# Optimization experiments

Hardware: AMD Instinct MI355X
Metric: run time of the kernel (lower is better)

## Reference

```python
import jax, jax.numpy as jnp
import numpy as np

N_INT = 16384
N_BND = 4096
DIM_X = 3
NUM_RES = 8
NUM_FC = 3
D = 128


def _dim_net(x, wf, bf, Wres, bres, Wl, bl, lo, hi):
    # x: scalar coordinate for one input dimension; returns scalar u-component
    h = (2.0 * (x - lo) / (hi - lo) - 1.0) * wf + bf  # fc_first: Linear(1,D) -> [D]

    def block(h, p):
        W, b = p  # W: [NUM_FC, D, D], b: [NUM_FC, D]
        g = h
        for l in range(NUM_FC):
            g = g @ W[l] + b[l]
            if l != NUM_FC - 1:
                g = jnp.sin(g)
        return jnp.sin(g + h), None

    h, _ = jax.lax.scan(block, h, (Wres, bres))
    return (h @ Wl + bl)[0]  # fc_last: Linear(D,1) -> scalar


_d2_net = jax.grad(jax.grad(_dim_net, argnums=0), argnums=0)

# vmap over points (axis 0 of x) then over dims (axis 1 of X / axis 0 of params)
_vals = jax.vmap(jax.vmap(_dim_net, in_axes=(0,) + (None,) * 8),
                 in_axes=(1,) + (0,) * 8)
_d2s = jax.vmap(jax.vmap(_d2_net, in_axes=(0,) + (None,) * 8),
                in_axes=(1,) + (0,) * 8)


def setup_inputs() -> dict:
    key = jax.random.key(0)
    ks = jax.random.split(key, 5)
    X = jax.random.uniform(ks[0], (N_INT + N_BND, DIM_X), dtype=jnp.float32)
    rhs = jax.random.normal(ks[1], (N_INT + N_BND, 1), dtype=jnp.float32)
    w_first = 0.2 * jax.random.normal(ks[2], (DIM_X, D), dtype=jnp.float32)
    b_first = jnp.zeros((DIM_X, D), jnp.float32)
    W_res = jax.random.normal(ks[3], (DIM_X, NUM_RES, NUM_FC, D, D),
                              dtype=jnp.float32) / jnp.sqrt(jnp.float32(D))
    b_res = jnp.zeros((DIM_X, NUM_RES, NUM_FC, D), jnp.float32)
    W_last = jax.random.normal(ks[4], (DIM_X, D, 1),
                               dtype=jnp.float32) / jnp.sqrt(jnp.float32(D))
    b_last = jnp.zeros((DIM_X, 1), jnp.float32)
    lb = jnp.zeros((DIM_X,), jnp.float32)
    ub = jnp.ones((DIM_X,), jnp.float32)
    return {"X": X, "rhs": rhs, "w_first": w_first, "b_first": b_first,
            "W_res": W_res, "b_res": b_res, "W_last": W_last, "b_last": b_last,
            "lb": lb, "ub": ub}


def reference(X, rhs, w_first, b_first, W_res, b_res, W_last, b_last, lb, ub):
    Xi = X[:N_INT]          # interior points
    Xb = X[N_INT:]          # boundary points

    # Separable network: u(x) = prod_i f_i(x_i), so
    # Laplace u = sum_i f_i''(x_i) * prod_{j!=i} f_j(x_j)  (same math as double autograd)
    F = _vals(Xi, w_first, b_first, W_res, b_res, W_last, b_last, lb, ub)   # [DIM_X, N_INT]
    F2 = _d2s(Xi, w_first, b_first, W_res, b_res, W_last, b_last, lb, ub)   # [DIM_X, N_INT]

    lap = jnp.zeros_like(F[0])
    for i in range(DIM_X):
        p = F2[i]
        for j in range(DIM_X):
            if j != i:
                p = p * F[j]
        lap = lap + p

    equation = -lap[:, None] - rhs[:N_INT]

    Fb = _vals(Xb, w_first, b_first, W_res, b_res, W_last, b_last, lb, ub)  # [DIM_X, N_BND]
    u_b = jnp.prod(Fb, axis=0)[:, None]
    boundary = u_b - rhs[N_INT:]
    return equation, boundary
```

## Files before the change

### kernel.cpp

```cpp
#include <hip/hip_runtime.h>

#define N_INT 16384
#define NPTS  20480
#define DIMX  3
#define NRES  8
#define NFC   3
#define DD    128
#define Q     8
#define WPW   4
#define TPB   (WPW*64)
#define TILES_PER_DIM (NPTS/Q)
#define INT_TILES     (N_INT/Q)
#define NLAYER (DIMX*NRES*NFC)
#define MT 2
#define NT 8
#define KS 4

typedef unsigned int   u32;
typedef unsigned short u16;
typedef _Float16 f16;
typedef f16   f16x8 __attribute__((ext_vector_type(8)));
typedef float f32x4 __attribute__((ext_vector_type(4)));
typedef float v2f   __attribute__((ext_vector_type(2)));
typedef float v4f   __attribute__((ext_vector_type(4)));

__device__ __forceinline__ u32 pack_split(float x) {
    f16 h = (f16)x;
    f16 l = (f16)(x - (float)h);
    union { f16 f; u16 u; } a, b;
    a.f = h; b.f = l;
    return (u32)a.u | ((u32)b.u << 16);
}

__device__ __forceinline__ int aidx(int row, int feat) {
    return row*DD + (feat ^ (((row >> 1) & 7) << 3));
}

#define PKFMA_LO(ACC, W2, X2) \
  asm("v_pk_fma_f32 %0, %1, %2, %0 op_sel:[0,0,0] op_sel_hi:[1,0,1]" \
      : "+v"(ACC) : "v"(W2), "v"(X2))
#define PKFMA_HI(ACC, W2, X2) \
  asm("v_pk_fma_f32 %0, %1, %2, %0 op_sel:[0,1,0] op_sel_hi:[1,1,1]" \
      : "+v"(ACC) : "v"(W2), "v"(X2))

__global__ void pack_w(const float* __restrict__ W_res,
                       f16* __restrict__ Whi, f16* __restrict__ Wlo)
{
    int t = blockIdx.x*256 + threadIdx.x;
    if (t >= NLAYER*KS*NT*64) return;
    int lane = t & 63;
    int nt   = (t >> 6) & 7;
    int ks   = (t >> 9) & 3;
    int L    = t >> 11;
    int n = nt*16 + (lane & 15);
    size_t src = (size_t)L*DD*DD + (size_t)(ks*32 + (lane >> 4)*8)*DD + n;
    f16x8 vh, vl;
#pragma unroll
    for (int i = 0; i < 8; ++i) {
        float w = W_res[src + (size_t)i*DD];
        f16 hh = (f16)w;
        vh[i] = hh;
        vl[i] = (f16)(w - (float)hh);
    }
    ((f16x8*)Whi)[t] = vh;
    ((f16x8*)Wlo)[t] = vl;
}

__global__ __launch_bounds__(TPB, 2) void pinn_main(
    const float* __restrict__ X,
    const float* __restrict__ w_first,
    const float* __restrict__ b_first,
    const float* __restrict__ W_res,
    const float* __restrict__ b_res,
    const float* __restrict__ W_last,
    const float* __restrict__ b_last,
    const float* __restrict__ lb,
    const float* __restrict__ ub,
    const f16* __restrict__ Whi,
    const f16* __restrict__ Wlo,
    float* __restrict__ Fout,
    float* __restrict__ F2out)
{
    __shared__ u32 ldsA[WPW][32*DD];
    const int wave = threadIdx.x >> 6;
    const int lane = threadIdx.x & 63;
    const int gw   = blockIdx.x * WPW + wave;
    const int dim  = gw / TILES_PER_DIM;
    const int tile = gw % TILES_PER_DIM;
    const int p0   = tile * Q;

    const float lo = lb[dim], hi = ub[dim];
    const float sc = 2.0f / (hi - lo);
    const float blv = b_last[dim];
    const float* bp0 = b_res + (size_t)dim*(NRES*NFC*DD);

    if (tile < INT_TILES) {
        u32* A = ldsA[wave];
        const int g = lane >> 4;
        const int c = lane & 15;
        const f16x8* WHp = (const f16x8*)Whi;
        const f16x8* WLp = (const f16x8*)Wlo;

        float hv_[MT][NT], hd_[MT][NT], hdd_[MT][NT];
        float wfv[NT], bfv[NT], blw[NT];
        float tq[MT];
#pragma unroll
        for (int mt = 0; mt < MT; ++mt) {
            int q = 4*mt + g;
            float x = X[(p0 + q)*DIMX + dim];
            tq[mt] = fmaf(x - lo, sc, -1.0f);
        }
#pragma unroll
        for (int nt = 0; nt < NT; ++nt) {
            int f = nt*16 + c;
            wfv[nt] = w_first[dim*DD + f];
            bfv[nt] = b_first[dim*DD + f];
            blw[nt] = W_last[dim*DD + f];
        }
#pragma unroll
        for (int mt = 0; mt < MT; ++mt)
#pragma unroll
            for (int nt = 0; nt < NT; ++nt) {
                hv_[mt][nt]  = fmaf(tq[mt], wfv[nt], bfv[nt]);
                hd_[mt][nt]  = sc * wfv[nt];
                hdd_[mt][nt] = 0.f;
            }

        const int Lbase = dim * NRES * NFC;
        const float* bp = bp0;

#pragma unroll 1
        for (int r = 0; r < NRES; ++r) {
#pragma unroll
            for (int mt = 0; mt < MT; ++mt)
#pragma unroll
                for (int nt = 0; nt < NT; ++nt) {
                    int row = mt*16 + 4*g;
                    int f   = nt*16 + c;
                    A[aidx(row+0, f)] = pack_split(hv_[mt][nt]);
                    A[aidx(row+1, f)] = pack_split(hd_[mt][nt]);
                    A[aidx(row+2, f)] = pack_split(hdd_[mt][nt]);
                }

#pragma unroll 1
            for (int l = 0; l < NFC; ++l) {
                const int L = Lbase + r*NFC + l;
                f32x4 acc[MT][NT];
#pragma unroll
                for (int mt = 0; mt < MT; ++mt)
#pragma unroll
                    for (int nt = 0; nt < NT; ++nt)
                        acc[mt][nt] = (f32x4){0.f, 0.f, 0.f, 0.f};

#pragma unroll 1
                for (int ks = 0; ks < KS; ++ks) {
                    f16x8 ah[MT], al[MT];
#pragma unroll
                    for (int mt = 0; mt < MT; ++mt) {
                        int idx = aidx(mt*16 + c, ks*32 + g*8);
                        const uint4 A0 = *(const uint4*)&A[idx];
                        const uint4 A1 = *(const uint4*)&A[idx + 4];
                        union { u32 u[4]; f16x8 v; } ch, cl;
                        ch.u[0] = (A0.x & 0xFFFFu) | (A0.y << 16);
                        ch.u[1] = (A0.z & 0xFFFFu) | (A0.w << 16);
                        ch.u[2] = (A1.x & 0xFFFFu) | (A1.y << 16);
                        ch.u[3] = (A1.z & 0xFFFFu) | (A1.w << 16);
                        cl.u[0] = (A0.x >> 16) | (A0.y & 0xFFFF0000u);
                        cl.u[1] = (A0.z >> 16) | (A0.w & 0xFFFF0000u);
                        cl.u[2] = (A1.x >> 16) | (A1.y & 0xFFFF0000u);
                        cl.u[3] = (A1.z >> 16) | (A1.w & 0xFFFF0000u);
                        ah[mt] = ch.v;  al[mt] = cl.v;
                    }
                    const f16x8* whb = WHp + (size_t)((L*KS + ks)*NT)*64;
                    const f16x8* wlb = WLp + (size_t)((L*KS + ks)*NT)*64;
#pragma unroll
                    for (int nt = 0; nt < NT; ++nt) {
                        f16x8 bh = whb[nt*64 + lane];
                        f16x8 bl = wlb[nt*64 + lane];
#pragma unroll
                        for (int mt = 0; mt < MT; ++mt) {
                            acc[mt][nt] = __builtin_amdgcn_mfma_f32_16x16x32_f16(ah[mt], bh, acc[mt][nt], 0, 0, 0);
                            acc[mt][nt] = __builtin_amdgcn_mfma_f32_16x16x32_f16(al[mt], bh, acc[mt][nt], 0, 0, 0);
                            acc[mt][nt] = __builtin_amdgcn_mfma_f32_16x16x32_f16(ah[mt], bl, acc[mt][nt], 0, 0, 0);
                        }
                    }
                }

                float bia[NT];
#pragma unroll
                for (int nt = 0; nt < NT; ++nt) bia[nt] = bp[nt*16 + c];

                if (l < NFC-1) {
#pragma unroll
                    for (int mt = 0; mt < MT; ++mt)
#pragma unroll
                        for (int nt = 0; nt < NT; ++nt) {
                            float a0 = acc[mt][nt][0] + bia[nt];
                            float a1 = acc[mt][nt][1];
                            float a2 = acc[mt][nt][2];
                            float s  = __sinf(a0);
                            float cs = __cosf(a0);
                            float nv  = s;
                            float nd2 = fmaf(cs, a2, -s*a1*a1);
                            float nd1 = cs*a1;
                            int row = mt*16 + 4*g;
                            int f   = nt*16 + c;
                            A[aidx(row+0, f)] = pack_split(nv);
                            A[aidx(row+1, f)] = pack_split(nd1);
                            A[aidx(row+2, f)] = pack_split(nd2);
                        }
                } else {
#pragma unroll
                    for (int mt = 0; mt < MT; ++mt)
#pragma unroll
                        for (int nt = 0; nt < NT; ++nt) {
                            float zu = acc[mt][nt][0] + bia[nt] + hv_[mt][nt];
                            float z1 = acc[mt][nt][1] + hd_[mt][nt];
                            float z2 = acc[mt][nt][2] + hdd_[mt][nt];
                            float s  = __sinf(zu);
                            float cs = __cosf(zu);
                            hv_[mt][nt]  = s;
                            hd_[mt][nt]  = cs*z1;
                            hdd_[mt][nt] = fmaf(cs, z2, -s*z1*z1);
                        }
                }
                bp += DD;
            }
        }

#pragma unroll
        for (int mt = 0; mt < MT; ++mt) {
            float pv = 0.f, p2 = 0.f;
#pragma unroll
            for (int nt = 0; nt < NT; ++nt) {
                pv = fmaf(hv_[mt][nt],  blw[nt], pv);
                p2 = fmaf(hdd_[mt][nt], blw[nt], p2);
            }
#pragma unroll
            for (int off = 1; off < 16; off <<= 1) {
                pv += __shfl_xor(pv, off);
                p2 += __shfl_xor(p2, off);
            }
            if (c == 0) {
                int q = 4*mt + g;
                Fout [dim*NPTS + p0 + q] = pv + blv;
                F2out[dim*NPTS + p0 + q] = p2;
            }
        }
    } else {
        float* Af = (float*)ldsA[wave];
        const int d0 = lane * 2;
        const float wf0 = w_first[dim*DD + d0];
        const float wf1 = w_first[dim*DD + d0 + 1];
        const float bf0 = b_first[dim*DD + d0];
        const float bf1 = b_first[dim*DD + d0 + 1];
        const float wl0 = W_last[dim*DD + d0];
        const float wl1 = W_last[dim*DD + d0 + 1];

        float hv[Q][2];
#pragma unroll
        for (int q = 0; q < Q; ++q) {
            float x = X[(p0 + q)*DIMX + dim];
            float t = fmaf(x - lo, sc, -1.0f);
            hv[q][0] = fmaf(t, wf0, bf0);
            hv[q][1] = fmaf(t, wf1, bf1);
        }

        const float* Wp = W_res + (size_t)dim*(NRES*NFC*DD*DD);
        const float* bp = bp0;

#pragma unroll 1
        for (int r = 0; r < NRES; ++r) {
#pragma unroll
            for (int q = 0; q < Q; ++q)
                *(float2*)&Af[q*DD + d0] = make_float2(hv[q][0], hv[q][1]);

#pragma unroll 1
            for (int l = 0; l < NFC; ++l) {
                v2f av[Q];
#pragma unroll
                for (int q = 0; q < Q; ++q) av[q] = (v2f){0.f, 0.f};
                const float* WL = Wp;
#pragma unroll 1
                for (int k0 = 0; k0 < DD; k0 += 4) {
                    const float* wr = WL + k0*DD + d0;
                    const v2f w0 = *(const v2f*)(wr);
                    const v2f w1 = *(const v2f*)(wr + DD);
                    const v2f w2 = *(const v2f*)(wr + 2*DD);
                    const v2f w3 = *(const v2f*)(wr + 3*DD);
#pragma unroll
                    for (int q = 0; q < Q; ++q) {
                        const v4f x0 = *(const v4f*)&Af[q*DD + k0];
                        const v2f x0a = x0.lo, x0b = x0.hi;
                        PKFMA_LO(av[q], w0, x0a);
                        PKFMA_HI(av[q], w1, x0a);
                        PKFMA_LO(av[q], w2, x0b);
                        PKFMA_HI(av[q], w3, x0b);
                    }
                }
                const float bv0 = bp[d0], bv1 = bp[d0+1];
#pragma unroll
                for (int q = 0; q < Q; ++q) av[q] += (v2f){bv0, bv1};

                if (l < NFC-1) {
#pragma unroll
                    for (int q = 0; q < Q; ++q)
                        *(float2*)&Af[q*DD + d0] =
                            make_float2(__sinf(av[q].x), __sinf(av[q].y));
                } else {
#pragma unroll
                    for (int q = 0; q < Q; ++q) {
                        hv[q][0] = __sinf(av[q].x + hv[q][0]);
                        hv[q][1] = __sinf(av[q].y + hv[q][1]);
                    }
                }
                Wp += DD*DD;
                bp += DD;
            }
        }

#pragma unroll
        for (int q = 0; q < Q; ++q) {
            float pv = fmaf(hv[q][0], wl0, hv[q][1]*wl1);
#pragma unroll
            for (int off = 32; off > 0; off >>= 1)
                pv += __shfl_down(pv, off);
            if (lane == 0)
                Fout[dim*NPTS + p0 + q] = pv + blv;
        }
    }
}

__global__ void pinn_combine(const float* __restrict__ F, const float* __restrict__ F2,
                             const float* __restrict__ rhs, float* __restrict__ out)
{
    int n = blockIdx.x*256 + threadIdx.x;
    if (n >= NPTS) return;
    float f0 = F[n], f1 = F[NPTS+n], f2 = F[2*NPTS+n];
    if (n < N_INT) {
        float lap = F2[n]*f1*f2 + F2[NPTS+n]*f0*f2 + F2[2*NPTS+n]*f0*f1;
        out[n] = -lap - rhs[n];
    } else {
        out[n] = f0*f1*f2 - rhs[n];
    }
}

extern "C" void kernel_launch(void* const* d_in, const int* in_sizes, int n_in,
                              void* d_out, int out_size, void* d_ws, size_t ws_size,
                              hipStream_t stream) {
    const float* X       = (const float*)d_in[0];
    const float* rhs     = (const float*)d_in[1];
    const float* w_first = (const float*)d_in[2];
    const float* b_first = (const float*)d_in[3];
    const float* W_res   = (const float*)d_in[4];
    const float* b_res   = (const float*)d_in[5];
    const float* W_last  = (const float*)d_in[6];
    const float* b_last  = (const float*)d_in[7];
    const float* lbv     = (const float*)d_in[8];
    const float* ubv     = (const float*)d_in[9];
    float* out = (float*)d_out;

    float* F  = (float*)d_ws;
    float* F2 = F + 3*NPTS;
    f16*   Whi = (f16*)((char*)d_ws + (size_t)6*NPTS*4);
    f16*   Wlo = Whi + (size_t)NLAYER*KS*NT*64*8;

    int wpthreads = NLAYER*KS*NT*64;
    pack_w<<<(wpthreads + 255)/256, 256, 0, stream>>>(W_res, Whi, Wlo);

    int wgs = DIMX * TILES_PER_DIM / WPW;
    pinn_main<<<wgs, TPB, 0, stream>>>(X, w_first, b_first, W_res, b_res,
                                       W_last, b_last, lbv, ubv, Whi, Wlo, F, F2);
    pinn_combine<<<(NPTS+255)/256, 256, 0, stream>>>(F, F2, rhs, out);
}
```

Before: 1.011 ms.

## Compact LDS activation rows to cut shared memory and raise occupancy

The per-wave LDS activation buffer drops from 32 rows to 25 by storing only the three used rows (value, first and second derivative) per point. The unused fourth row of each MFMA group is redirected to a single shared zero/padding row. The swizzle pattern changes to match the new row packing, and launch bounds go from 2 to 3 blocks per SIMD so the smaller LDS footprint can fit more waves. The tighter register budget from the higher launch bound may cause spills. Padding row 24 must also hold zeros for the MFMA results to stay correct.

```diff
diff --git a/kernel.cpp b/kernel.cpp
--- a/kernel.cpp
+++ b/kernel.cpp
@@ -15,6 +15,7 @@
 #define MT 2
 #define NT 8
 #define KS 4
+#define LROWS 25
 
 typedef unsigned int   u32;
 typedef unsigned short u16;
@@ -33,7 +34,7 @@
 }
 
 __device__ __forceinline__ int aidx(int row, int feat) {
-    return row*DD + (feat ^ (((row >> 1) & 7) << 3));
+    return row*DD + (feat ^ ((row & 7) << 2));
 }
 
 #define PKFMA_LO(ACC, W2, X2) \
@@ -66,7 +67,7 @@
     ((f16x8*)Wlo)[t] = vl;
 }
 
-__global__ __launch_bounds__(TPB, 2) void pinn_main(
+__global__ __launch_bounds__(TPB, 3) void pinn_main(
     const float* __restrict__ X,
     const float* __restrict__ w_first,
     const float* __restrict__ b_first,
@@ -81,7 +82,7 @@
     float* __restrict__ Fout,
     float* __restrict__ F2out)
 {
-    __shared__ u32 ldsA[WPW][32*DD];
+    __shared__ u32 ldsA[WPW][LROWS*DD];
     const int wave = threadIdx.x >> 6;
     const int lane = threadIdx.x & 63;
     const int gw   = blockIdx.x * WPW + wave;
@@ -101,6 +102,10 @@
         const f16x8* WHp = (const f16x8*)Whi;
         const f16x8* WLp = (const f16x8*)Wlo;
 
+        const int c3 = c & 3;
+        const int Rr0 = (c3 == 3) ? 24 : (3*(c >> 2) + c3);
+        const int Rr1 = (c3 == 3) ? 24 : (12 + 3*(c >> 2) + c3);
+
         float hv_[MT][NT], hd_[MT][NT], hdd_[MT][NT];
         float wfv[NT], bfv[NT], blw[NT];
         float tq[MT];
@@ -135,11 +140,11 @@
             for (int mt = 0; mt < MT; ++mt)
 #pragma unroll
                 for (int nt = 0; nt < NT; ++nt) {
-                    int row = mt*16 + 4*g;
-                    int f   = nt*16 + c;
-                    A[aidx(row+0, f)] = pack_split(hv_[mt][nt]);
-                    A[aidx(row+1, f)] = pack_split(hd_[mt][nt]);
-                    A[aidx(row+2, f)] = pack_split(hdd_[mt][nt]);
+                    int R = 12*mt + 3*g;
+                    int f = nt*16 + c;
+                    A[aidx(R+0, f)] = pack_split(hv_[mt][nt]);
+                    A[aidx(R+1, f)] = pack_split(hd_[mt][nt]);
+                    A[aidx(R+2, f)] = pack_split(hdd_[mt][nt]);
                 }
 
 #pragma unroll 1
@@ -154,12 +159,13 @@
 
 #pragma unroll 1
                 for (int ks = 0; ks < KS; ++ks) {
+                    const int kb = ks*32 + g*8;
                     f16x8 ah[MT], al[MT];
 #pragma unroll
                     for (int mt = 0; mt < MT; ++mt) {
-                        int idx = aidx(mt*16 + c, ks*32 + g*8);
-                        const uint4 A0 = *(const uint4*)&A[idx];
-                        const uint4 A1 = *(const uint4*)&A[idx + 4];
+                        const int R = mt ? Rr1 : Rr0;
+                        const uint4 A0 = *(const uint4*)&A[aidx(R, kb)];
+                        const uint4 A1 = *(const uint4*)&A[aidx(R, kb + 4)];
                         union { u32 u[4]; f16x8 v; } ch, cl;
                         ch.u[0] = (A0.x & 0xFFFFu) | (A0.y << 16);
                         ch.u[1] = (A0.z & 0xFFFFu) | (A0.w << 16);
@@ -203,11 +209,11 @@
                             float nv  = s;
                             float nd2 = fmaf(cs, a2, -s*a1*a1);
                             float nd1 = cs*a1;
-                            int row = mt*16 + 4*g;
-                            int f   = nt*16 + c;
-                            A[aidx(row+0, f)] = pack_split(nv);
-                            A[aidx(row+1, f)] = pack_split(nd1);
-                            A[aidx(row+2, f)] = pack_split(nd2);
+                            int R = 12*mt + 3*g;
+                            int f = nt*16 + c;
+                            A[aidx(R+0, f)] = pack_split(nv);
+                            A[aidx(R+1, f)] = pack_split(nd1);
+                            A[aidx(R+2, f)] = pack_split(nd2);
                         }
                 } else {
 #pragma unroll
```

Measured after the change: 1.261 ms. 1.25x slower.
